# Kernel optimization log

Measured on AMD Instinct MI355X. Metric: run time of the kernel, lower is better.

## Reference

```python
import jax, jax.numpy as jnp
import numpy as np

N = 50000
E = 500000
HID = 64
HEADS = 4
LAYERS = 4
CDIM = 8


def _p(key, shape, scale=0.05):
    return jax.random.normal(key, shape, dtype=jnp.float32) * scale


def setup_inputs() -> dict:
    key = jax.random.key(0)
    ks = jax.random.split(key, 32)
    x = jax.random.normal(ks[0], (N, 8), dtype=jnp.float32)
    src = jax.random.randint(ks[1], (E,), 0, N)
    dst = jax.random.randint(ks[2], (E,), 0, N)
    edge_index = jnp.stack([src, dst]).astype(jnp.int64)
    HC = HEADS * HID
    inp = {
        "x": x,
        "edge_index": edge_index,
        # encoder: Linear(8,64), ELU, Linear(64,64), ELU
        "enc_w1": _p(ks[3], (HID, 8)), "enc_b1": _p(ks[4], (HID,)),
        "enc_w2": _p(ks[5], (HID, HID)), "enc_b2": _p(ks[6], (HID,)),
        # per-layer TransformerConv params, stacked over layers
        "Wq": _p(ks[7], (LAYERS, HC, HID)), "bq": _p(ks[8], (LAYERS, HC)),
        "Wk": _p(ks[9], (LAYERS, HC, HID)), "bk": _p(ks[10], (LAYERS, HC)),
        "Wv": _p(ks[11], (LAYERS, HC, HID)), "bv": _p(ks[12], (LAYERS, HC)),
        "Ws": _p(ks[13], (LAYERS, HID, HID)), "bs": _p(ks[14], (LAYERS, HID)),
        # output MLP: 64->64->32->8
        "out_w1": _p(ks[15], (64, HID)), "out_b1": _p(ks[16], (64,)),
        "out_w2": _p(ks[17], (32, 64)), "out_b2": _p(ks[18], (32,)),
        "out_w3": _p(ks[19], (CDIM, 32)), "out_b3": _p(ks[20], (CDIM,)),
    }
    return inp


def transformer_conv(h, src, dst, Wq, bq, Wk, bk, Wv, bv, Ws, bs):
    """PyG TransformerConv, concat=False, root_weight=True, eval mode (no dropout)."""
    n = h.shape[0]
    q = (h @ Wq.T + bq).reshape(n, HEADS, HID)
    k = (h @ Wk.T + bk).reshape(n, HEADS, HID)
    v = (h @ Wv.T + bv).reshape(n, HEADS, HID)
    # per-edge multi-head scores: (E, H)
    alpha = jnp.einsum("ehd,ehd->eh", q[dst], k[src]) / np.sqrt(HID).astype(np.float32)
    # segment softmax over edges grouped by destination node
    amax = jax.ops.segment_max(alpha, dst, num_segments=n)          # (N, H)
    ex = jnp.exp(alpha - amax[dst])                                 # (E, H)
    denom = jax.ops.segment_sum(ex, dst, num_segments=n)           # (N, H)
    w = ex / denom[dst]                                             # (E, H)
    msg = v[src] * w[:, :, None]                                    # (E, H, C)
    agg = jax.ops.segment_sum(msg, dst, num_segments=n)            # (N, H, C)
    out = agg.mean(axis=1)                                          # concat=False -> head mean
    return out + h @ Ws.T + bs                                      # skip connection


def reference(x, edge_index, enc_w1, enc_b1, enc_w2, enc_b2,
              Wq, bq, Wk, bk, Wv, bv, Ws, bs,
              out_w1, out_b1, out_w2, out_b2, out_w3, out_b3):
    src, dst = edge_index[0], edge_index[1]
    elu = jax.nn.elu
    h = elu(x @ enc_w1.T + enc_b1)
    h = elu(h @ enc_w2.T + enc_b2)
    for l in range(LAYERS):
        h = elu(transformer_conv(h, src, dst, Wq[l], bq[l], Wk[l], bk[l],
                                 Wv[l], bv[l], Ws[l], bs[l]))
        # dropout is identity in eval mode
    o = elu(h @ out_w1.T + out_b1)
    o = elu(o @ out_w2.T + out_b2)
    o = o @ out_w3.T + out_b3
    return o
```

## Files before the change

kernel.cpp:

```cpp
#include <hip/hip_runtime.h>
#include <hip/hip_bf16.h>

#define N_NODES 50000
#define N_EDGES 500000
constexpr int HID = 64;
constexpr int HC  = 256;

typedef unsigned short u16;
typedef unsigned char u8;
typedef __attribute__((ext_vector_type(8))) __bf16 bf16x8;
typedef __attribute__((ext_vector_type(4))) float f32x4;
typedef __attribute__((ext_vector_type(2))) float f32x2;

__device__ __forceinline__ float b2f(u16 u) {
    union { unsigned int i; float f; } c; c.i = ((unsigned int)u) << 16; return c.f;
}
__device__ __forceinline__ u16 f2b(float f) {
    union { float f; unsigned int i; } c; c.f = f;
    unsigned int x = c.i;
    unsigned int lsb = (x >> 16) & 1u;
    x += 0x7fffu + lsb;
    return (u16)(x >> 16);
}
__device__ __forceinline__ float elu_f(float x) { return x > 0.f ? x : expm1f(x); }


__global__ __launch_bounds__(256) void detect_kernel(const int* __restrict__ ei, int* __restrict__ flag) {
    __shared__ int s[4];
    int t = threadIdx.x;
    int nz = ei[2 * t + 1] != 0;
    unsigned long long m = __ballot(nz);
    if ((t & 63) == 0) s[t >> 6] = (m != 0ull) ? 1 : 0;
    __syncthreads();
    if (t == 0) flag[0] = s[0] | s[1] | s[2] | s[3];
}

__global__ __launch_bounds__(256) void wcvt_kernel(const float* __restrict__ Wq, const float* __restrict__ Wk,
                                                   const float* __restrict__ Wv, const float* __restrict__ Wsk,
                                                   u16* __restrict__ w16) {
    int i = blockIdx.x * 256 + threadIdx.x;
    if (i >= 53248) return;
    const float* src; int off;
    if (i < 16384)      { src = Wq;  off = i; }
    else if (i < 32768) { src = Wk;  off = i - 16384; }
    else if (i < 49152) { src = Wv;  off = i - 32768; }
    else                { src = Wsk; off = i - 49152; }
    float4 v = ((const float4*)src)[off];
    ushort4 u; u.x = f2b(v.x); u.y = f2b(v.y); u.z = f2b(v.z); u.w = f2b(v.w);
    ((ushort4*)w16)[i] = u;
}

__global__ __launch_bounds__(256) void hist_kernel(const int* __restrict__ ei, const int* __restrict__ flag,
                                                   int* __restrict__ cnt) {
    int e = blockIdx.x * 256 + threadIdx.x;
    if (e < N_EDGES) {
        int d = flag[0] ? ei[N_EDGES + e] : ei[2 * N_EDGES + 2 * e];
        atomicAdd(&cnt[d], 1);
    }
}

__global__ __launch_bounds__(512) void scan1_kernel(const int* __restrict__ cnt,
                                                    int* __restrict__ row_start, int* __restrict__ bsum) {
    __shared__ int sc[512];
    int t = threadIdx.x;
    int i = blockIdx.x * 512 + t;
    int v = (i < N_NODES) ? cnt[i] : 0;
    sc[t] = v;
    __syncthreads();
    for (int off = 1; off < 512; off <<= 1) {
        int u = (t >= off) ? sc[t - off] : 0;
        __syncthreads();
        sc[t] += u;
        __syncthreads();
    }
    if (i < N_NODES) row_start[i] = sc[t] - v;
    if (t == 511) bsum[blockIdx.x] = sc[511];
}

__global__ __launch_bounds__(128) void scan2_kernel(int* __restrict__ bsum, int* __restrict__ row_start) {
    __shared__ int sc[128];
    const int NB = (N_NODES + 511) / 512;
    int t = threadIdx.x;
    int v = (t < NB) ? bsum[t] : 0;
    sc[t] = v;
    __syncthreads();
    for (int off = 1; off < 128; off <<= 1) {
        int u = (t >= off) ? sc[t - off] : 0;
        __syncthreads();
        sc[t] += u;
        __syncthreads();
    }
    if (t < NB) bsum[t] = sc[t] - v;
    if (t == 127) row_start[N_NODES] = sc[127];
}

__global__ __launch_bounds__(512) void scan3_kernel(int* __restrict__ row_start, const int* __restrict__ bsum) {
    int i = blockIdx.x * 512 + threadIdx.x;
    if (i < N_NODES) row_start[i] += bsum[blockIdx.x];
}

__global__ __launch_bounds__(256) void scatter_kernel(const int* __restrict__ ei, const int* __restrict__ flag,
                                const int* __restrict__ row_start, int* __restrict__ cursor,
                                int* __restrict__ csr_src) {
    int e = blockIdx.x * 256 + threadIdx.x;
    if (e < N_EDGES) {
        int isI32 = flag[0];
        int s = isI32 ? ei[e] : ei[2 * e];
        int d = isI32 ? ei[N_EDGES + e] : ei[2 * N_EDGES + 2 * e];
        int pos = row_start[d] + atomicAdd(&cursor[d], 1);
        csr_src[pos] = s;
    }
}

__global__ __launch_bounds__(256) void encoder_kernel(const float* __restrict__ x,
                               const float* __restrict__ w1, const float* __restrict__ b1,
                               const float* __restrict__ w2, const float* __restrict__ b2,
                               u16* __restrict__ h) {
    __shared__ float xs[64 * 9];
    __shared__ float w1s[64 * 9];
    __shared__ u16 t1s[64 * 72];
    __shared__ u16 w2s[64 * 72];
    __shared__ float b1s[64], b2s[64];
    int t = threadIdx.x;
    int m0 = blockIdx.x * 64;

    if (t < 128) {
        int row = t >> 1, c = (t & 1) * 4;
        float4 val = make_float4(0.f, 0.f, 0.f, 0.f);
        if (m0 + row < N_NODES) val = *(const float4*)(x + (size_t)(m0 + row) * 8 + c);
        *(float4*)&xs[row * 9 + c] = val;
    }
    if (t >= 128 && t < 256) {
        int p = t - 128;
        int row = p >> 1, c = (p & 1) * 4;
        float4 val = *(const float4*)(w1 + row * 8 + c);
        *(float4*)&w1s[row * 9 + c] = val;
    }
    #pragma unroll
    for (int r = 0; r < 4; ++r) {
        int p = t + r * 256; int row = p >> 4, kc = (p & 15) * 4;
        float4 val = *(const float4*)(w2 + row * 64 + kc);
        ushort4 u; u.x = f2b(val.x); u.y = f2b(val.y); u.z = f2b(val.z); u.w = f2b(val.w);
        *(ushort4*)&w2s[row * 72 + kc] = u;
    }
    if (t < 64) { b1s[t] = b1[t]; b2s[t] = b2[t]; }
    __syncthreads();

    {
        int j = t & 63, sub = t >> 6;
        #pragma unroll
        for (int g = 0; g < 16; ++g) {
            int node = g * 4 + sub;
            float acc = b1s[j];
            #pragma unroll
            for (int m = 0; m < 8; ++m) acc += xs[node * 9 + m] * w1s[j * 9 + m];
            t1s[node * 72 + j] = f2b(elu_f(acc));
        }
    }
    __syncthreads();

    int wave = t >> 6, lane = t & 63;
    int lrow = lane & 15, quad = lane >> 4;
    int m_off = wave * 16;
    bf16x8 a0 = *(const bf16x8*)&t1s[(m_off + lrow) * 72 + quad * 8];
    bf16x8 a1 = *(const bf16x8*)&t1s[(m_off + lrow) * 72 + 32 + quad * 8];
    #pragma unroll
    for (int nsub = 0; nsub < 4; ++nsub) {
        bf16x8 b0 = *(const bf16x8*)&w2s[(nsub * 16 + lrow) * 72 + quad * 8];
        bf16x8 b1v = *(const bf16x8*)&w2s[(nsub * 16 + lrow) * 72 + 32 + quad * 8];
        f32x4 acc = {0.f, 0.f, 0.f, 0.f};
        acc = __builtin_amdgcn_mfma_f32_16x16x32_bf16(a0, b0, acc, 0, 0, 0);
        acc = __builtin_amdgcn_mfma_f32_16x16x32_bf16(a1, b1v, acc, 0, 0, 0);
        int col = nsub * 16 + lrow;
        float bias = b2s[col];
        #pragma unroll
        for (int r = 0; r < 4; ++r) {
            int row = m0 + m_off + quad * 4 + r;
            if (row < N_NODES) h[(size_t)row * 64 + col] = f2b(elu_f(acc[r] + bias));
        }
    }
}

__global__ __launch_bounds__(256) void proj_kernel(const u16* __restrict__ h,
    const u16* __restrict__ wq16, const u16* __restrict__ wk16,
    const u16* __restrict__ wv16, const u16* __restrict__ wsk16,
    const float* __restrict__ bq, const float* __restrict__ bk,
    const float* __restrict__ bv, const float* __restrict__ bsk,
    int layer,
    u8* __restrict__ qv, u8* __restrict__ kv, u16* __restrict__ skip)
{
    __shared__ u16 wsA[64 * 72];
    __shared__ u16 wsB[64 * 72];
    __shared__ __align__(16) u8 poolraw[128 * 144];
    u8*  qst  = poolraw;
    u8*  kvst = poolraw;
    u16* skst = (u16*)poolraw;

    int t = threadIdx.x;
    int m0 = blockIdx.x * 128;
    int wave = t >> 6, lane = t & 63;
    int lrow = lane & 15, quad = lane >> 4;
    int nl0 = wave * 16 + lrow;
    int nl1 = 64 + nl0;

    const u16* Wq16  = wq16  + (size_t)layer * HC * HID;
    const u16* Wk16  = wk16  + (size_t)layer * HC * HID;
    const u16* Wv16  = wv16  + (size_t)layer * HC * HID;
    const u16* Wsk16 = wsk16 + (size_t)layer * HID * HID;
    const float* bqL  = bq  + layer * HC;
    const float* bkL  = bk  + layer * HC;
    const float* bvL  = bv  + layer * HC;
    const float* bskL = bsk + layer * HID;

    auto stageIssue = [&](const u16* W, int cb, uint4& r0, uint4& r1) {
        const u16* sp = W + (size_t)(cb + (t >> 3)) * 64 + (t & 7) * 8;
        r0 = *(const uint4*)sp;
        r1 = *(const uint4*)(sp + 2048);
    };
    auto stageWrite = [&](u16* buf, uint4 r0, uint4 r1) {
        int row = t >> 3, kc = (t & 7) * 8;
        *(uint4*)&buf[row * 72 + kc] = r0;
        *(uint4*)&buf[(row + 32) * 72 + kc] = r1;
    };

    uint4 hv[4];
    #pragma unroll
    for (int it = 0; it < 4; ++it) {
        int p = t + it * 256; int row = p >> 3, kc = (p & 7) * 8;
        hv[it] = make_uint4(0u, 0u, 0u, 0u);
        if (m0 + row < N_NODES) hv[it] = *(const uint4*)(h + (size_t)(m0 + row) * 64 + kc);
    }
    uint4 q0r0, q0r1;
    stageIssue(Wq16, 0, q0r0, q0r1);
    #pragma unroll
    for (int it = 0; it < 4; ++it) {
        int p = t + it * 256; int row = p >> 3, kc = (p & 7) * 8;
        if (row < 64) *(uint4*)&wsA[row * 72 + kc] = hv[it];
        else          *(uint4*)&wsB[(row - 64) * 72 + kc] = hv[it];
    }
    __syncthreads();
    bf16x8 a0 = *(const bf16x8*)&wsA[nl0 * 72 + quad * 8];
    bf16x8 a1 = *(const bf16x8*)&wsA[nl0 * 72 + 32 + quad * 8];
    bf16x8 a2 = *(const bf16x8*)&wsB[nl0 * 72 + quad * 8];
    bf16x8 a3 = *(const bf16x8*)&wsB[nl0 * 72 + 32 + quad * 8];
    __syncthreads();
    stageWrite(wsB, q0r0, q0r1);
    __syncthreads();

    auto computeQ = [&](int ct, const u16* BUF) {
        #pragma unroll
        for (int nsub = 0; nsub < 4; ++nsub) {
            bf16x8 w0 = *(const bf16x8*)&BUF[(nsub * 16 + lrow) * 72 + quad * 8];
            bf16x8 w1 = *(const bf16x8*)&BUF[(nsub * 16 + lrow) * 72 + 32 + quad * 8];
            float4 b4 = *(const float4*)(bqL + ct * 64 + nsub * 16 + quad * 4);
            int c4 = nsub * 16 + quad * 4;
            f32x4 acc = {0.f, 0.f, 0.f, 0.f};
            acc = __builtin_amdgcn_mfma_f32_16x16x32_bf16(w0, a0, acc, 0, 0, 0);
            acc = __builtin_amdgcn_mfma_f32_16x16x32_bf16(w1, a1, acc, 0, 0, 0);
            {
                float f0 = (acc[0] + b4.x) * 16.f, f1 = (acc[1] + b4.y) * 16.f;
                float f2v = (acc[2] + b4.z) * 16.f, f3v = (acc[3] + b4.w) * 16.f;
                int pk = __builtin_amdgcn_cvt_pk_fp8_f32(f0, f1, 0, false);
                pk = __builtin_amdgcn_cvt_pk_fp8_f32(f2v, f3v, pk, true);
                *(unsigned int*)&qst[nl0 * 80 + c4] = (unsigned int)pk;
            }
            f32x4 acc2 = {0.f, 0.f, 0.f, 0.f};
            acc2 = __builtin_amdgcn_mfma_f32_16x16x32_bf16(w0, a2, acc2, 0, 0, 0);
            acc2 = __builtin_amdgcn_mfma_f32_16x16x32_bf16(w1, a3, acc2, 0, 0, 0);
            {
                float f0 = (acc2[0] + b4.x) * 16.f, f1 = (acc2[1] + b4.y) * 16.f;
                float f2v = (acc2[2] + b4.z) * 16.f, f3v = (acc2[3] + b4.w) * 16.f;
                int pk = __builtin_amdgcn_cvt_pk_fp8_f32(f0, f1, 0, false);
                pk = __builtin_amdgcn_cvt_pk_fp8_f32(f2v, f3v, pk, true);
                *(unsigned int*)&qst[nl1 * 80 + c4] = (unsigned int)pk;
            }
        }
    };
    auto computeKV = [&](int ct, const u16* BUF, const float* bias, int voff) {
        #pragma unroll
        for (int nsub = 0; nsub < 4; ++nsub) {
            bf16x8 w0 = *(const bf16x8*)&BUF[(nsub * 16 + lrow) * 72 + quad * 8];
            bf16x8 w1 = *(const bf16x8*)&BUF[(nsub * 16 + lrow) * 72 + 32 + quad * 8];
            float4 b4 = *(const float4*)(bias + ct * 64 + nsub * 16 + quad * 4);
            int g = nsub * 4 + quad;
            f32x4 acc = {0.f, 0.f, 0.f, 0.f};
            acc = __builtin_amdgcn_mfma_f32_16x16x32_bf16(w0, a0, acc, 0, 0, 0);
            acc = __builtin_amdgcn_mfma_f32_16x16x32_bf16(w1, a1, acc, 0, 0, 0);
            {
                float f0 = (acc[0] + b4.x) * 16.f, f1 = (acc[1] + b4.y) * 16.f;
                float f2v = (acc[2] + b4.z) * 16.f, f3v = (acc[3] + b4.w) * 16.f;
                int pk = __builtin_amdgcn_cvt_pk_fp8_f32(f0, f1, 0, false);
                pk = __builtin_amdgcn_cvt_pk_fp8_f32(f2v, f3v, pk, true);
                *(unsigned int*)&kvst[nl0 * 144 + g * 8 + voff] = (unsigned int)pk;
            }
            f32x4 acc2 = {0.f, 0.f, 0.f, 0.f};
            acc2 = __builtin_amdgcn_mfma_f32_16x16x32_bf16(w0, a2, acc2, 0, 0, 0);
            acc2 = __builtin_amdgcn_mfma_f32_16x16x32_bf16(w1, a3, acc2, 0, 0, 0);
            {
                float f0 = (acc2[0] + b4.x) * 16.f, f1 = (acc2[1] + b4.y) * 16.f;
                float f2v = (acc2[2] + b4.z) * 16.f, f3v = (acc2[3] + b4.w) * 16.f;
                int pk = __builtin_amdgcn_cvt_pk_fp8_f32(f0, f1, 0, false);
                pk = __builtin_amdgcn_cvt_pk_fp8_f32(f2v, f3v, pk, true);
                *(unsigned int*)&kvst[nl1 * 144 + g * 8 + voff] = (unsigned int)pk;
            }
        }
    };
    auto computeSK = [&](const u16* BUF) {
        #pragma unroll
        for (int nsub = 0; nsub < 4; ++nsub) {
            bf16x8 w0 = *(const bf16x8*)&BUF[(nsub * 16 + lrow) * 72 + quad * 8];
            bf16x8 w1 = *(const bf16x8*)&BUF[(nsub * 16 + lrow) * 72 + 32 + quad * 8];
            float4 b4 = *(const float4*)(bskL + nsub * 16 + quad * 4);
            int c4 = nsub * 16 + quad * 4;
            f32x4 acc = {0.f, 0.f, 0.f, 0.f};
            acc = __builtin_amdgcn_mfma_f32_16x16x32_bf16(w0, a0, acc, 0, 0, 0);
            acc = __builtin_amdgcn_mfma_f32_16x16x32_bf16(w1, a1, acc, 0, 0, 0);
            ushort4 s4;
            s4.x = f2b(acc[0] + b4.x); s4.y = f2b(acc[1] + b4.y);
            s4.z = f2b(acc[2] + b4.z); s4.w = f2b(acc[3] + b4.w);
            *(ushort4*)&skst[nl0 * 72 + c4] = s4;
            f32x4 acc2 = {0.f, 0.f, 0.f, 0.f};
            acc2 = __builtin_amdgcn_mfma_f32_16x16x32_bf16(w0, a2, acc2, 0, 0, 0);
            acc2 = __builtin_amdgcn_mfma_f32_16x16x32_bf16(w1, a3, acc2, 0, 0, 0);
            ushort4 s5;
            s5.x = f2b(acc2[0] + b4.x); s5.y = f2b(acc2[1] + b4.y);
            s5.z = f2b(acc2[2] + b4.z); s5.w = f2b(acc2[3] + b4.w);
            *(ushort4*)&skst[nl1 * 72 + c4] = s5;
        }
    };
    auto flushQ = [&](int ct) {
        #pragma unroll
        for (int it = 0; it < 2; ++it) {
            int p = t + it * 256; int row = p >> 2, ch = p & 3;
            int grow = m0 + row;
            if (grow < N_NODES)
                *(uint4*)(qv + (size_t)grow * 256 + ct * 64 + ch * 16) = *(const uint4*)&qst[row * 80 + ch * 16];
        }
    };
    auto flushKV = [&](int ct) {
        #pragma unroll
        for (int it = 0; it < 4; ++it) {
            int p = t + it * 256; int row = p >> 3, ch = p & 7;
            int grow = m0 + row;
            if (grow < N_NODES)
                *(uint4*)(kv + (size_t)grow * 512 + ct * 128 + ch * 16) = *(const uint4*)&kvst[row * 144 + ch * 16];
        }
    };

    uint4 r0, r1;
    stageIssue(Wq16, 64, r0, r1);  computeQ(0, wsB);          __syncthreads(); flushQ(0);  stageWrite(wsA, r0, r1); __syncthreads();
    stageIssue(Wq16, 128, r0, r1); computeQ(1, wsA);          __syncthreads(); flushQ(1);  stageWrite(wsB, r0, r1); __syncthreads();
    stageIssue(Wq16, 192, r0, r1); computeQ(2, wsB);          __syncthreads(); flushQ(2);  stageWrite(wsA, r0, r1); __syncthreads();
    stageIssue(Wk16, 0, r0, r1);   computeQ(3, wsA);          __syncthreads(); flushQ(3);  stageWrite(wsB, r0, r1); __syncthreads();
    stageIssue(Wv16, 0, r0, r1);   computeKV(0, wsB, bkL, 0); __syncthreads();             stageWrite(wsA, r0, r1); __syncthreads();
    stageIssue(Wk16, 64, r0, r1);  computeKV(0, wsA, bvL, 4); __syncthreads(); flushKV(0); stageWrite(wsB, r0, r1); __syncthreads();
    stageIssue(Wv16, 64, r0, r1);  computeKV(1, wsB, bkL, 0); __syncthreads();             stageWrite(wsA, r0, r1); __syncthreads();
    stageIssue(Wk16, 128, r0, r1); computeKV(1, wsA, bvL, 4); __syncthreads(); flushKV(1); stageWrite(wsB, r0, r1); __syncthreads();
    stageIssue(Wv16, 128, r0, r1); computeKV(2, wsB, bkL, 0); __syncthreads();             stageWrite(wsA, r0, r1); __syncthreads();
    stageIssue(Wk16, 192, r0, r1); computeKV(2, wsA, bvL, 4); __syncthreads(); flushKV(2); stageWrite(wsB, r0, r1); __syncthreads();
    stageIssue(Wv16, 192, r0, r1); computeKV(3, wsB, bkL, 0); __syncthreads();             stageWrite(wsA, r0, r1); __syncthreads();
    stageIssue(Wsk16, 0, r0, r1);  computeKV(3, wsA, bvL, 4); __syncthreads(); flushKV(3); stageWrite(wsB, r0, r1); __syncthreads();

    computeSK(wsB);
    __syncthreads();
    #pragma unroll
    for (int it = 0; it < 4; ++it) {
        int p = t + it * 256; int row = p >> 3, ch = p & 7;
        int grow = m0 + row;
        if (grow < N_NODES)
            *(uint4*)(skip + (size_t)grow * 64 + ch * 8) = *(const uint4*)&skst[row * 72 + ch * 8];
    }
}

#define DPP_ADD(x, ctrl) ((x) + __builtin_bit_cast(float, \
    __builtin_amdgcn_update_dpp(0, __builtin_bit_cast(int, (x)), (ctrl), 0xf, 0xf, true)))

#define ATTN_QUAD(S0q, S1q, S2q, S3q, V1, V2, V3) do { \
    uint2 c0 = *(const uint2*)(kvl + (size_t)(unsigned)(S0q) * 512); \
    uint2 c1 = *(const uint2*)(kvl + (size_t)(unsigned)(S1q) * 512); \
    uint2 c2 = *(const uint2*)(kvl + (size_t)(unsigned)(S2q) * 512); \
    uint2 c3 = *(const uint2*)(kvl + (size_t)(unsigned)(S3q) * 512); \
    f32x2 k0a = __builtin_amdgcn_cvt_pk_f32_fp8(c0.x, false), k0b = __builtin_amdgcn_cvt_pk_f32_fp8(c0.x, true); \
    f32x2 k1a = __builtin_amdgcn_cvt_pk_f32_fp8(c1.x, false), k1b = __builtin_amdgcn_cvt_pk_f32_fp8(c1.x, true); \
    f32x2 k2a = __builtin_amdgcn_cvt_pk_f32_fp8(c2.x, false), k2b = __builtin_amdgcn_cvt_pk_f32_fp8(c2.x, true); \
    f32x2 k3a = __builtin_amdgcn_cvt_pk_f32_fp8(c3.x, false), k3b = __builtin_amdgcn_cvt_pk_f32_fp8(c3.x, true); \
    f32x2 pd0 = qlo * k0a + qhi * k0b; \
    f32x2 pd1 = qlo * k1a + qhi * k1b; \
    f32x2 pd2 = qlo * k2a + qhi * k2b; \
    f32x2 pd3 = qlo * k3a + qhi * k3b; \
    float p0 = pd0.x + pd0.y, p1 = pd1.x + pd1.y, p2 = pd2.x + pd2.y, p3 = pd3.x + pd3.y; \
    p0 = DPP_ADD(p0, 0xB1);  p1 = DPP_ADD(p1, 0xB1);  p2 = DPP_ADD(p2, 0xB1);  p3 = DPP_ADD(p3, 0xB1);  \
    p0 = DPP_ADD(p0, 0x4E);  p1 = DPP_ADD(p1, 0x4E);  p2 = DPP_ADD(p2, 0x4E);  p3 = DPP_ADD(p3, 0x4E);  \
    p0 = DPP_ADD(p0, 0x141); p1 = DPP_ADD(p1, 0x141); p2 = DPP_ADD(p2, 0x141); p3 = DPP_ADD(p3, 0x141); \
    p0 = DPP_ADD(p0, 0x140); p1 = DPP_ADD(p1, 0x140); p2 = DPP_ADD(p2, 0x140); p3 = DPP_ADD(p3, 0x140); \
    float w0 = __expf(p0 * SC); \
    float w1 = (V1) ? __expf(p1 * SC) : 0.f; \
    float w2 = (V2) ? __expf(p2 * SC) : 0.f; \
    float w3 = (V3) ? __expf(p3 * SC) : 0.f; \
    l += (w0 + w1) + (w2 + w3); \
    f32x2 v0a = __builtin_amdgcn_cvt_pk_f32_fp8(c0.y, false), v0b = __builtin_amdgcn_cvt_pk_f32_fp8(c0.y, true); \
    f32x2 v1a = __builtin_amdgcn_cvt_pk_f32_fp8(c1.y, false), v1b = __builtin_amdgcn_cvt_pk_f32_fp8(c1.y, true); \
    f32x2 v2a = __builtin_amdgcn_cvt_pk_f32_fp8(c2.y, false), v2b = __builtin_amdgcn_cvt_pk_f32_fp8(c2.y, true); \
    f32x2 v3a = __builtin_amdgcn_cvt_pk_f32_fp8(c3.y, false), v3b = __builtin_amdgcn_cvt_pk_f32_fp8(c3.y, true); \
    accA += v0a * w0; accA += v1a * w1; accA += v2a * w2; accA += v3a * w3; \
    accB += v0b * w0; accB += v1b * w1; accB += v2b * w2; accB += v3b * w3; \
} while (0)

__global__ __launch_bounds__(256) void attn_kernel(
    const u8* __restrict__ q, const u8* __restrict__ kv,
    const u16* __restrict__ skip,
    const int* __restrict__ row_start, const int* __restrict__ csr_src,
    u16* __restrict__ hout)
{
    __shared__ int s_lds[4][64];
    int wave = threadIdx.x >> 6;
    int lane = threadIdx.x & 63;
    int n = blockIdx.x * 4 + wave;
    if (n >= N_NODES) return;
    unsigned qw = ((const unsigned*)(q + (size_t)n * 256))[lane];
    f32x2 qlo = __builtin_amdgcn_cvt_pk_f32_fp8(qw, false);
    f32x2 qhi = __builtin_amdgcn_cvt_pk_f32_fp8(qw, true);
    ushort4 sk4 = make_ushort4(0, 0, 0, 0);
    if ((lane >> 4) == 0) sk4 = ((const ushort4*)(skip + (size_t)n * 64))[lane];
    const u8* kvl = kv + lane * 8;
    const float SC = 4.8828125e-4f;
    float l = 0.f;
    f32x2 accA = {0.f, 0.f};
    f32x2 accB = {0.f, 0.f};
    int e0 = row_start[n];
    int deg = row_start[n + 1] - e0;

    for (int base = 0; base < deg; base += 64) {
        int rem = deg - base;
        int m = rem < 64 ? rem : 64;
        int li = lane < m ? lane : m - 1;
        s_lds[wave][lane] = csr_src[e0 + base + li];
        int i = 0;
        for (; i + 4 <= m; i += 4) {
            int4 sq = *(const int4*)&s_lds[wave][i];
            ATTN_QUAD(sq.x, sq.y, sq.z, sq.w, 1, 1, 1);
        }
        if (i < m) {
            int4 sq = *(const int4*)&s_lds[wave][i];
            int rem2 = m - i;
            int sB = rem2 > 1 ? sq.y : sq.x;
            int sC = rem2 > 2 ? sq.z : sq.x;
            ATTN_QUAD(sq.x, sB, sC, sq.x, rem2 > 1, rem2 > 2, 0);
        }
    }

    float inv = l > 0.f ? 1.f / l : 0.f;
    float a0 = accA.x * inv, a1 = accA.y * inv;
    float a2 = accB.x * inv, a3 = accB.y * inv;
    a0 += __shfl_xor(a0, 16); a0 += __shfl_xor(a0, 32);
    a1 += __shfl_xor(a1, 16); a1 += __shfl_xor(a1, 32);
    a2 += __shfl_xor(a2, 16); a2 += __shfl_xor(a2, 32);
    a3 += __shfl_xor(a3, 16); a3 += __shfl_xor(a3, 32);
    if ((lane >> 4) == 0) {
        const float OS = 0.015625f;
        ushort4 o;
        o.x = f2b(elu_f(OS * a0 + b2f(sk4.x)));
        o.y = f2b(elu_f(OS * a1 + b2f(sk4.y)));
        o.z = f2b(elu_f(OS * a2 + b2f(sk4.z)));
        o.w = f2b(elu_f(OS * a3 + b2f(sk4.w)));
        ((ushort4*)(hout + (size_t)n * 64))[lane] = o;
    }
}

__global__ __launch_bounds__(256) void mlp_kernel(const u16* __restrict__ h,
    const float* __restrict__ w1, const float* __restrict__ b1,
    const float* __restrict__ w2, const float* __restrict__ b2,
    const float* __restrict__ w3, const float* __restrict__ b3,
    float* __restrict__ out)
{
    __shared__ u16 hs[64 * 72];
    __shared__ u16 w1s[64 * 72];
    __shared__ u16 t1s[64 * 72];
    __shared__ u16 w2s[32 * 72];
    __shared__ float t2s[64 * 33];
    __shared__ float w3s[8 * 33];
    __shared__ float b1s[64], b2s[32], b3s[8];
    int t = threadIdx.x;
    int m0 = blockIdx.x * 64;

    #pragma unroll
    for (int it = 0; it < 2; ++it) {
        int p = t + it * 256; int row = p >> 3, kc = (p & 7) * 8;
        uint4 val = make_uint4(0u, 0u, 0u, 0u);
        if (m0 + row < N_NODES) val = *(const uint4*)(h + (size_t)(m0 + row) * 64 + kc);
        *(uint4*)&hs[row * 72 + kc] = val;
    }
    #pragma unroll
    for (int r = 0; r < 4; ++r) {
        int p = t + r * 256; int row = p >> 4, kc = (p & 15) * 4;
        float4 val = *(const float4*)(w1 + row * 64 + kc);
        ushort4 u; u.x = f2b(val.x); u.y = f2b(val.y); u.z = f2b(val.z); u.w = f2b(val.w);
        *(ushort4*)&w1s[row * 72 + kc] = u;
    }
    #pragma unroll
    for (int r = 0; r < 2; ++r) {
        int p = t + r * 256; int row = p >> 4, kc = (p & 15) * 4;
        float4 val = *(const float4*)(w2 + row * 64 + kc);
        ushort4 u; u.x = f2b(val.x); u.y = f2b(val.y); u.z = f2b(val.z); u.w = f2b(val.w);
        *(ushort4*)&w2s[row * 72 + kc] = u;
    }
    if (t < 8 * 32) { int r = t >> 5, c = t & 31; w3s[r * 33 + c] = w3[t]; }
    if (t < 64) b1s[t] = b1[t];
    if (t >= 64 && t < 96) b2s[t - 64] = b2[t - 64];
    if (t >= 96 && t < 104) b3s[t - 96] = b3[t - 96];
    __syncthreads();

    int wave = t >> 6, lane = t & 63;
    int lrow = lane & 15, quad = lane >> 4;
    int m_off = wave * 16;

    {
        bf16x8 a0 = *(const bf16x8*)&hs[(m_off + lrow) * 72 + quad * 8];
        bf16x8 a1 = *(const bf16x8*)&hs[(m_off + lrow) * 72 + 32 + quad * 8];
        #pragma unroll
        for (int nsub = 0; nsub < 4; ++nsub) {
            bf16x8 b0 = *(const bf16x8*)&w1s[(nsub * 16 + lrow) * 72 + quad * 8];
            bf16x8 b1v = *(const bf16x8*)&w1s[(nsub * 16 + lrow) * 72 + 32 + quad * 8];
            f32x4 acc = {0.f, 0.f, 0.f, 0.f};
            acc = __builtin_amdgcn_mfma_f32_16x16x32_bf16(a0, b0, acc, 0, 0, 0);
            acc = __builtin_amdgcn_mfma_f32_16x16x32_bf16(a1, b1v, acc, 0, 0, 0);
            int col = nsub * 16 + lrow;
            float bias = b1s[col];
            #pragma unroll
            for (int r = 0; r < 4; ++r) {
                int row = m_off + quad * 4 + r;
                t1s[row * 72 + col] = f2b(elu_f(acc[r] + bias));
            }
        }
    }
    __syncthreads();

    {
        bf16x8 a0 = *(const bf16x8*)&t1s[(m_off + lrow) * 72 + quad * 8];
        bf16x8 a1 = *(const bf16x8*)&t1s[(m_off + lrow) * 72 + 32 + quad * 8];
        #pragma unroll
        for (int nsub = 0; nsub < 2; ++nsub) {
            bf16x8 b0 = *(const bf16x8*)&w2s[(nsub * 16 + lrow) * 72 + quad * 8];
            bf16x8 b1v = *(const bf16x8*)&w2s[(nsub * 16 + lrow) * 72 + 32 + quad * 8];
            f32x4 acc = {0.f, 0.f, 0.f, 0.f};
            acc = __builtin_amdgcn_mfma_f32_16x16x32_bf16(a0, b0, acc, 0, 0, 0);
            acc = __builtin_amdgcn_mfma_f32_16x16x32_bf16(a1, b1v, acc, 0, 0, 0);
            int col = nsub * 16 + lrow;
            float bias = b2s[col];
            #pragma unroll
            for (int r = 0; r < 4; ++r) {
                int row = m_off + quad * 4 + r;
                t2s[row * 33 + col] = elu_f(acc[r] + bias);
            }
        }
    }
    __syncthreads();

    #pragma unroll
    for (int r = 0; r < 2; ++r) {
        int idx = t + r * 256;
        int node = idx >> 3, j = idx & 7;
        int row = m0 + node;
        if (row < N_NODES) {
            float acc = b3s[j];
            #pragma unroll
            for (int kk = 0; kk < 32; ++kk) acc += t2s[node * 33 + kk] * w3s[j * 33 + kk];
            out[(size_t)row * 8 + j] = acc;
        }
    }
}

extern "C" void kernel_launch(void* const* d_in, const int* in_sizes, int n_in,
                              void* d_out, int out_size, void* d_ws, size_t ws_size,
                              hipStream_t stream) {
    (void)in_sizes; (void)n_in; (void)out_size; (void)ws_size;
    const float* x   = (const float*)d_in[0];
    const int* ei    = (const int*)d_in[1];
    const float* ew1 = (const float*)d_in[2];
    const float* eb1 = (const float*)d_in[3];
    const float* ew2 = (const float*)d_in[4];
    const float* eb2 = (const float*)d_in[5];
    const float* Wq  = (const float*)d_in[6];
    const float* bq  = (const float*)d_in[7];
    const float* Wk  = (const float*)d_in[8];
    const float* bk  = (const float*)d_in[9];
    const float* Wv  = (const float*)d_in[10];
    const float* bv  = (const float*)d_in[11];
    const float* Wsk = (const float*)d_in[12];
    const float* bsk = (const float*)d_in[13];
    const float* ow1 = (const float*)d_in[14];
    const float* ob1 = (const float*)d_in[15];
    const float* ow2 = (const float*)d_in[16];
    const float* ob2 = (const float*)d_in[17];
    const float* ow3 = (const float*)d_in[18];
    const float* ob3 = (const float*)d_in[19];

    char* ws = (char*)d_ws;
    size_t off = 0;
    auto alloc = [&](size_t bytes) -> void* {
        void* p = ws + off;
        off += (bytes + 255) & ~(size_t)255;
        return p;
    };
    u16*   h0    = (u16*)  alloc((size_t)N_NODES * 64 * 2);
    u16*   h1    = (u16*)  alloc((size_t)N_NODES * 64 * 2);
    u8*    q     = (u8*)   alloc((size_t)N_NODES * 256);
    u8*    kv    = (u8*)   alloc((size_t)N_NODES * 512);
    u16*   skp   = (u16*)  alloc((size_t)N_NODES * 64 * 2);
    u16*   w16   = (u16*)  alloc((size_t)212992 * 2);
    int*   cnt   = (int*)  alloc((size_t)N_NODES * 4);
    int*   cursor= (int*)  alloc((size_t)N_NODES * 4);
    int*   rowst = (int*)  alloc((size_t)(N_NODES + 1) * 4);
    int*   csr   = (int*)  alloc((size_t)N_EDGES * 4);
    int*   bsum  = (int*)  alloc(512);
    int*   flag  = (int*)  alloc(256);

    u16* wq16  = w16;
    u16* wk16  = w16 + 65536;
    u16* wv16  = w16 + 131072;
    u16* wsk16 = w16 + 196608;

    const int NB = (N_NODES + 511) / 512;

    hipMemsetAsync(cnt, 0, 2 * 200192, stream);
    detect_kernel<<<1, 256, 0, stream>>>(ei, flag);
    wcvt_kernel<<<208, 256, 0, stream>>>(Wq, Wk, Wv, Wsk, w16);
    hist_kernel<<<(N_EDGES + 255) / 256, 256, 0, stream>>>(ei, flag, cnt);
    scan1_kernel<<<NB, 512, 0, stream>>>(cnt, rowst, bsum);
    scan2_kernel<<<1, 128, 0, stream>>>(bsum, rowst);
    scan3_kernel<<<NB, 512, 0, stream>>>(rowst, bsum);
    scatter_kernel<<<(N_EDGES + 255) / 256, 256, 0, stream>>>(ei, flag, rowst, cursor, csr);

    encoder_kernel<<<(N_NODES + 63) / 64, 256, 0, stream>>>(x, ew1, eb1, ew2, eb2, h0);

    u16* hin = h0;
    u16* hout = h1;
    for (int l = 0; l < 4; ++l) {
        proj_kernel<<<(N_NODES + 127) / 128, 256, 0, stream>>>(hin, wq16, wk16, wv16, wsk16,
                                                               bq, bk, bv, bsk, l, q, kv, skp);
        attn_kernel<<<(N_NODES + 3) / 4, 256, 0, stream>>>(q, kv, skp, rowst, csr, hout);
        u16* tmp = hin; hin = hout; hout = tmp;
    }

    mlp_kernel<<<(N_NODES + 63) / 64, 256, 0, stream>>>(hin, ow1, ob1, ow2, ob2, ow3, ob3, (float*)d_out);
}
```

Measured before the change: 416.8 us.

## Merge three-pass scan into single-block scan and restructure projection staging

Replaces the three-kernel prefix scan with a single 1024-thread block in which each thread serially sums 49 counts, so two kernel launches and the block-sum round trip go away. The projection kernel's K/V phase now stages the K and V weight tiles together into both shared buffers and computes them back to back, instead of alternating double-buffered stages that overlapped the next global load with the current compute. This cuts the number of barriers but gives up the load/compute overlap for the K/V and skip weights. The single-block scan also serialises work on one CU, and each thread reads strided addresses that do not coalesce.

```diff
diff --git a/kernel.cpp b/kernel.cpp
--- a/kernel.cpp
+++ b/kernel.cpp
@@ -59,44 +59,33 @@
     }
 }
 
-__global__ __launch_bounds__(512) void scan1_kernel(const int* __restrict__ cnt,
-                                                    int* __restrict__ row_start, int* __restrict__ bsum) {
-    __shared__ int sc[512];
+__global__ __launch_bounds__(1024) void scan_kernel(const int* __restrict__ cnt, int* __restrict__ row_start) {
+    __shared__ int sc[1024];
+    const int PER = 49;
     int t = threadIdx.x;
-    int i = blockIdx.x * 512 + t;
-    int v = (i < N_NODES) ? cnt[i] : 0;
-    sc[t] = v;
-    __syncthreads();
-    for (int off = 1; off < 512; off <<= 1) {
+    int base = t * PER;
+    int sum = 0;
+    for (int j = 0; j < PER; ++j) {
+        int idx = base + j;
+        sum += (idx < N_NODES) ? cnt[idx] : 0;
+    }
+    sc[t] = sum;
+    __syncthreads();
+    for (int off = 1; off < 1024; off <<= 1) {
         int u = (t >= off) ? sc[t - off] : 0;
         __syncthreads();
         sc[t] += u;
         __syncthreads();
     }
-    if (i < N_NODES) row_start[i] = sc[t] - v;
-    if (t == 511) bsum[blockIdx.x] = sc[511];
-}
-
-__global__ __launch_bounds__(128) void scan2_kernel(int* __restrict__ bsum, int* __restrict__ row_start) {
-    __shared__ int sc[128];
-    const int NB = (N_NODES + 511) / 512;
-    int t = threadIdx.x;
-    int v = (t < NB) ? bsum[t] : 0;
-    sc[t] = v;
-    __syncthreads();
-    for (int off = 1; off < 128; off <<= 1) {
-        int u = (t >= off) ? sc[t - off] : 0;
-        __syncthreads();
-        sc[t] += u;
-        __syncthreads();
-    }
-    if (t < NB) bsum[t] = sc[t] - v;
-    if (t == 127) row_start[N_NODES] = sc[127];
-}
-
-__global__ __launch_bounds__(512) void scan3_kernel(int* __restrict__ row_start, const int* __restrict__ bsum) {
-    int i = blockIdx.x * 512 + threadIdx.x;
-    if (i < N_NODES) row_start[i] += bsum[blockIdx.x];
+    int run = (t > 0) ? sc[t - 1] : 0;
+    for (int j = 0; j < PER; ++j) {
+        int idx = base + j;
+        if (idx < N_NODES) {
+            row_start[idx] = run;
+            run += cnt[idx];
+        }
+    }
+    if (t == 1023) row_start[N_NODES] = sc[1023];
 }
 
 __global__ __launch_bounds__(256) void scatter_kernel(const int* __restrict__ ei, const int* __restrict__ flag,
@@ -348,27 +337,41 @@
     };
 
     uint4 r0, r1;
-    stageIssue(Wq16, 64, r0, r1);  computeQ(0, wsB);          __syncthreads(); flushQ(0);  stageWrite(wsA, r0, r1); __syncthreads();
-    stageIssue(Wq16, 128, r0, r1); computeQ(1, wsA);          __syncthreads(); flushQ(1);  stageWrite(wsB, r0, r1); __syncthreads();
-    stageIssue(Wq16, 192, r0, r1); computeQ(2, wsB);          __syncthreads(); flushQ(2);  stageWrite(wsA, r0, r1); __syncthreads();
-    stageIssue(Wk16, 0, r0, r1);   computeQ(3, wsA);          __syncthreads(); flushQ(3);  stageWrite(wsB, r0, r1); __syncthreads();
-    stageIssue(Wv16, 0, r0, r1);   computeKV(0, wsB, bkL, 0); __syncthreads();             stageWrite(wsA, r0, r1); __syncthreads();
-    stageIssue(Wk16, 64, r0, r1);  computeKV(0, wsA, bvL, 4); __syncthreads(); flushKV(0); stageWrite(wsB, r0, r1); __syncthreads();
-    stageIssue(Wv16, 64, r0, r1);  computeKV(1, wsB, bkL, 0); __syncthreads();             stageWrite(wsA, r0, r1); __syncthreads();
-    stageIssue(Wk16, 128, r0, r1); computeKV(1, wsA, bvL, 4); __syncthreads(); flushKV(1); stageWrite(wsB, r0, r1); __syncthreads();
-    stageIssue(Wv16, 128, r0, r1); computeKV(2, wsB, bkL, 0); __syncthreads();             stageWrite(wsA, r0, r1); __syncthreads();
-    stageIssue(Wk16, 192, r0, r1); computeKV(2, wsA, bvL, 4); __syncthreads(); flushKV(2); stageWrite(wsB, r0, r1); __syncthreads();
-    stageIssue(Wv16, 192, r0, r1); computeKV(3, wsB, bkL, 0); __syncthreads();             stageWrite(wsA, r0, r1); __syncthreads();
-    stageIssue(Wsk16, 0, r0, r1);  computeKV(3, wsA, bvL, 4); __syncthreads(); flushKV(3); stageWrite(wsB, r0, r1); __syncthreads();
-
-    computeSK(wsB);
-    __syncthreads();
-    #pragma unroll
-    for (int it = 0; it < 4; ++it) {
-        int p = t + it * 256; int row = p >> 3, ch = p & 7;
-        int grow = m0 + row;
-        if (grow < N_NODES)
-            *(uint4*)(skip + (size_t)grow * 64 + ch * 8) = *(const uint4*)&skst[row * 72 + ch * 8];
+    stageIssue(Wq16, 64, r0, r1);  computeQ(0, wsB); __syncthreads(); flushQ(0); stageWrite(wsA, r0, r1); __syncthreads();
+    stageIssue(Wq16, 128, r0, r1); computeQ(1, wsA); __syncthreads(); flushQ(1); stageWrite(wsB, r0, r1); __syncthreads();
+    stageIssue(Wq16, 192, r0, r1); computeQ(2, wsB); __syncthreads(); flushQ(2); stageWrite(wsA, r0, r1); __syncthreads();
+    computeQ(3, wsA); __syncthreads(); flushQ(3);
+
+    for (int ct = 0; ct < 4; ++ct) {
+        int cb = ct * 64;
+        uint4 k0, k1, v0, v1;
+        stageIssue(Wk16, cb, k0, k1);
+        stageIssue(Wv16, cb, v0, v1);
+        __syncthreads();
+        stageWrite(wsA, k0, k1);
+        stageWrite(wsB, v0, v1);
+        __syncthreads();
+        computeKV(ct, wsA, bkL, 0);
+        computeKV(ct, wsB, bvL, 4);
+        __syncthreads();
+        flushKV(ct);
+    }
+
+    {
+        uint4 s0, s1;
+        stageIssue(Wsk16, 0, s0, s1);
+        __syncthreads();
+        stageWrite(wsA, s0, s1);
+        __syncthreads();
+        computeSK(wsA);
+        __syncthreads();
+        #pragma unroll
+        for (int it = 0; it < 4; ++it) {
+            int p = t + it * 256; int row = p >> 3, ch = p & 7;
+            int grow = m0 + row;
+            if (grow < N_NODES)
+                *(uint4*)(skip + (size_t)grow * 64 + ch * 8) = *(const uint4*)&skst[row * 72 + ch * 8];
+        }
     }
 }
 
@@ -612,7 +615,6 @@
     int*   cursor= (int*)  alloc((size_t)N_NODES * 4);
     int*   rowst = (int*)  alloc((size_t)(N_NODES + 1) * 4);
     int*   csr   = (int*)  alloc((size_t)N_EDGES * 4);
-    int*   bsum  = (int*)  alloc(512);
     int*   flag  = (int*)  alloc(256);
 
     u16* wq16  = w16;
@@ -620,15 +622,11 @@
     u16* wv16  = w16 + 131072;
     u16* wsk16 = w16 + 196608;
 
-    const int NB = (N_NODES + 511) / 512;
-
     hipMemsetAsync(cnt, 0, 2 * 200192, stream);
     detect_kernel<<<1, 256, 0, stream>>>(ei, flag);
     wcvt_kernel<<<208, 256, 0, stream>>>(Wq, Wk, Wv, Wsk, w16);
     hist_kernel<<<(N_EDGES + 255) / 256, 256, 0, stream>>>(ei, flag, cnt);
-    scan1_kernel<<<NB, 512, 0, stream>>>(cnt, rowst, bsum);
-    scan2_kernel<<<1, 128, 0, stream>>>(bsum, rowst);
-    scan3_kernel<<<NB, 512, 0, stream>>>(rowst, bsum);
+    scan_kernel<<<1, 1024, 0, stream>>>(cnt, rowst);
     scatter_kernel<<<(N_EDGES + 255) / 256, 256, 0, stream>>>(ei, flag, rowst, cursor, csr);
 
     encoder_kernel<<<(N_NODES + 63) / 64, 256, 0, stream>>>(x, ew1, eb1, ew2, eb2, h0);
```

New measurement: 506.2 us. +21.4%, slower.
